# Optimization experiments

Hardware: AMD Instinct MI355X
Metric: run time of the kernel (lower is better)

## Reference

```python
import jax, jax.numpy as jnp
import numpy as np

BASE_C = 0.001
T = 0.7
MIN_RATIO = 0.5
MAX_RATIO = 2.0
EPS = 1e-7
BATCH, IN_DIM, HID, OUT_DIM = 65536, 784, 128, 10
WEIGHT_STD = 0.02


def _mobius_add(u, v, c):
    # (u +_c v) on the Poincare ball, last-dim vectors
    uv = jnp.sum(u * v, axis=-1, keepdims=True)
    uu = jnp.sum(u * u, axis=-1, keepdims=True)
    vv = jnp.sum(v * v, axis=-1, keepdims=True)
    num = (1.0 + 2.0 * c * uv + c * vv) * u + (1.0 - c * uu) * v
    den = 1.0 + 2.0 * c * uv + (c * c) * uu * vv
    return num / jnp.maximum(den, EPS)


def _mobius_scalar(x, c, r):
    # r (x)_c : tanh(r * artanh(sqrt(c)||x||)) * x / (sqrt(c)||x||)
    n = jnp.sqrt(jnp.maximum(jnp.sum(x * x, axis=-1, keepdims=True), EPS * EPS))
    sc = jnp.sqrt(c)
    arg = jnp.clip(sc * n, EPS, 1.0 - 1e-5)
    return jnp.tanh(r * jnp.arctanh(arg)) * x / (sc * n)


def poincare_ball_layer(h, u, c, t):
    # hyperbolic interpolation: ((1-t) (x)_c h) (+)_c (t (x)_c u)
    return _mobius_add(_mobius_scalar(h, c, 1.0 - t), _mobius_scalar(u, c, t), c)


def setup_inputs() -> dict:
    key = jax.random.key(0)
    ks = jax.random.split(key, 4)
    x = jax.random.normal(ks[0], (BATCH, IN_DIM), dtype=jnp.float32)
    weights1 = WEIGHT_STD * jax.random.normal(ks[1], (IN_DIM, HID), dtype=jnp.float32)
    bias1 = jnp.zeros((HID,), dtype=jnp.float32)
    weights2 = WEIGHT_STD * jax.random.normal(ks[2], (HID, HID), dtype=jnp.float32)
    bias2 = jnp.zeros((HID,), dtype=jnp.float32)
    out_weights = WEIGHT_STD * jax.random.normal(ks[3], (HID, OUT_DIM), dtype=jnp.float32)
    out_bias = jnp.zeros((OUT_DIM,), dtype=jnp.float32)
    curvature_scale = jnp.ones((1,), dtype=jnp.float32)
    return {"x": x, "weights1": weights1, "bias1": bias1, "weights2": weights2,
            "bias2": bias2, "out_weights": out_weights, "out_bias": out_bias,
            "curvature_scale": curvature_scale}


def reference(x, weights1, bias1, weights2, bias2, out_weights, out_bias, curvature_scale):
    x_flat = x.reshape(x.shape[0], -1)
    h = jnp.tanh(x_flat @ weights1 + bias1)            # [B, HID]
    u = jax.nn.sigmoid(h @ weights2 + bias2)           # [B, HID]
    # torch uses .item() -> curvature scale is detached from autodiff
    s = jax.lax.stop_gradient(jax.nn.sigmoid(curvature_scale[0]))
    adaptive_c = BASE_C * (MIN_RATIO + (MAX_RATIO - MIN_RATIO) * s)
    z = poincare_ball_layer(h, u, adaptive_c, T)
    z = jnp.where(jnp.any(jnp.isnan(z)), h, z)         # NaN fallback
    return z @ out_weights + out_bias
```

## Files before the change

kernel.cpp:

```cpp
#include <hip/hip_runtime.h>

typedef __attribute__((ext_vector_type(8))) short short8;
typedef __attribute__((ext_vector_type(4))) short short4v;
typedef __attribute__((ext_vector_type(4))) float f32x4;

#define BATCH 65536
#define IN_DIM 784
#define HID 128
#define OUT_DIM 10
#define KPAD 800
#define NKS 25
#define BM 128
#define NBLK (BATCH / BM)

#define OFF_W1H 0
#define OFF_W1L 204800
#define OFF_W2S 409600
#define OFF_W3S 442368

__device__ __forceinline__ unsigned short bf16_rne(float f) {
    unsigned u = __float_as_uint(f);
    return (unsigned short)((u + 0x7FFFu + ((u >> 16) & 1u)) >> 16);
}
__device__ __forceinline__ float fast_tanh(float x) {
    float e = __expf(2.0f * x);
    return 1.0f - 2.0f / (e + 1.0f);
}

__global__ void prep_kernel(const float* __restrict__ W1, const float* __restrict__ W2,
                            const float* __restrict__ W3,
                            unsigned short* __restrict__ w1h, unsigned short* __restrict__ w1l,
                            unsigned short* __restrict__ w2s, unsigned short* __restrict__ w3s) {
    int b = blockIdx.x, t = threadIdx.x;
    if (b < HID) {
        int col = b;
        for (int k = t; k < KPAD; k += 256) {
            float v = (k < IN_DIM) ? W1[k * HID + col] : 0.0f;
            unsigned u = __float_as_uint(v);
            unsigned short hi = (unsigned short)(u >> 16);
            float hif = __uint_as_float(u & 0xFFFF0000u);
            unsigned short lo = bf16_rne(v - hif);
            int idx = ((k >> 5) * HID + col) * 32 + (k & 31);
            w1h[idx] = hi; w1l[idx] = lo;
        }
    } else if (b == HID) {
        for (int i = t; i < HID * HID; i += 256) {
            int n = i >> 7, k = i & 127;
            w2s[i] = bf16_rne(W2[k * HID + n]);
        }
    } else {
        for (int i = t; i < 16 * HID; i += 256) {
            int j = i >> 7, k = i & 127;
            float v = (j < OUT_DIM) ? W3[k * OUT_DIM + j] : 0.0f;
            w3s[i] = bf16_rne(v);
        }
    }
}

__launch_bounds__(256, 2)
__global__ void fused_kernel(const float* __restrict__ X,
                             const float* __restrict__ b1,
                             const float* __restrict__ b2,
                             const float* __restrict__ ob,
                             const float* __restrict__ csc,
                             const unsigned short* __restrict__ w1h,
                             const unsigned short* __restrict__ w1l,
                             const unsigned short* __restrict__ w2s,
                             const unsigned short* __restrict__ w3s,
                             float* __restrict__ OUT) {
    __shared__ float xs[BM][36];
    __shared__ unsigned short w1hS[HID][40];
    __shared__ unsigned short w1lS[HID][40];
    __shared__ unsigned short ht[HID][136];

    const int t = threadIdx.x;
    const int wid = t >> 6, lane = t & 63;
    const int lg = lane >> 4, lr = lane & 15;
    const int row0 = blockIdx.x * BM;

    const float cs = csc[0];
    const float sgc = 1.0f / (1.0f + __expf(-cs));
    const float c = 0.001f * (0.5f + 1.5f * sgc);
    const float sc = sqrtf(c);

    f32x4 acc[2][8];
    #pragma unroll
    for (int f = 0; f < 8; ++f) {
        float bv = b1[16 * f + lr];
        f32x4 v = {bv, bv, bv, bv};
        acc[0][f] = v; acc[1][f] = v;
    }

    const int srow = t >> 1;
    const int shalf = t & 1;
    const float* xg = X + (size_t)(row0 + srow) * IN_DIM + shalf * 16;

    for (int ks = 0; ks < NKS; ++ks) {
        __syncthreads();
        {
            int k0 = ks * 32;
            f32x4 v0 = {0,0,0,0}, v1 = v0, v2 = v0, v3 = v0;
            if (k0 + shalf * 16 < IN_DIM) {
                const f32x4* p = (const f32x4*)(xg + k0);
                v0 = p[0]; v1 = p[1]; v2 = p[2]; v3 = p[3];
            }
            f32x4* q = (f32x4*)(&xs[srow][shalf * 16]);
            q[0] = v0; q[1] = v1; q[2] = v2; q[3] = v3;
        }
        {
            const short8* gh = (const short8*)(w1h + (ks * HID + srow) * 32 + shalf * 16);
            const short8* gl = (const short8*)(w1l + (ks * HID + srow) * 32 + shalf * 16);
            short8 h0 = gh[0], h1 = gh[1], l0 = gl[0], l1 = gl[1];
            short8* qh = (short8*)(&w1hS[srow][shalf * 16]);
            short8* ql = (short8*)(&w1lS[srow][shalf * 16]);
            qh[0] = h0; qh[1] = h1; ql[0] = l0; ql[1] = l1;
        }
        __syncthreads();

        short8 xh[2], xl[2];
        #pragma unroll
        for (int rf = 0; rf < 2; ++rf) {
            const int r = wid * 32 + rf * 16 + lr;
            const f32x4* p = (const f32x4*)(&xs[r][8 * lg]);
            f32x4 a = p[0], b = p[1];
            short8 h8, l8;
            #pragma unroll
            for (int j = 0; j < 8; ++j) {
                float v = (j < 4) ? a[j] : b[j - 4];
                unsigned u = __float_as_uint(v);
                h8[j] = (short)(u >> 16);
                float lof = v - __uint_as_float(u & 0xFFFF0000u);
                l8[j] = (short)(__float_as_uint(lof) >> 16);
            }
            xh[rf] = h8; xl[rf] = l8;
        }
        #pragma unroll
        for (int f = 0; f < 8; ++f) {
            const short8 bh = *(const short8*)(&w1hS[16 * f + lr][8 * lg]);
            const short8 bl = *(const short8*)(&w1lS[16 * f + lr][8 * lg]);
            acc[0][f] = __builtin_amdgcn_mfma_f32_16x16x32_bf16(xh[0], bh, acc[0][f], 0, 0, 0);
            acc[1][f] = __builtin_amdgcn_mfma_f32_16x16x32_bf16(xh[1], bh, acc[1][f], 0, 0, 0);
            acc[0][f] = __builtin_amdgcn_mfma_f32_16x16x32_bf16(xl[0], bh, acc[0][f], 0, 0, 0);
            acc[1][f] = __builtin_amdgcn_mfma_f32_16x16x32_bf16(xl[1], bh, acc[1][f], 0, 0, 0);
            acc[0][f] = __builtin_amdgcn_mfma_f32_16x16x32_bf16(xh[0], bl, acc[0][f], 0, 0, 0);
            acc[1][f] = __builtin_amdgcn_mfma_f32_16x16x32_bf16(xh[1], bl, acc[1][f], 0, 0, 0);
        }
    }

    #pragma unroll
    for (int rf = 0; rf < 2; ++rf) {
        const int rbase = wid * 32 + rf * 16 + 4 * lg;
        #pragma unroll
        for (int f = 0; f < 8; ++f) {
            short4v pk;
            #pragma unroll
            for (int r = 0; r < 4; ++r) {
                float h = fast_tanh(acc[rf][f][r]);
                acc[rf][f][r] = h;
                pk[r] = (short)bf16_rne(h);
            }
            *(short4v*)(&ht[16 * f + lr][rbase]) = pk;
        }
    }

    f32x4 uacc[2][8];
    #pragma unroll
    for (int f = 0; f < 8; ++f) {
        float bv = b2[16 * f + lr];
        f32x4 v = {bv, bv, bv, bv};
        uacc[0][f] = v; uacc[1][f] = v;
    }
    #pragma unroll
    for (int ks2 = 0; ks2 < 4; ++ks2) {
        short8 a2[2];
        #pragma unroll
        for (int rf = 0; rf < 2; ++rf) {
            const int rbl = wid * 32 + rf * 16 + lr;
            #pragma unroll
            for (int i = 0; i < 8; ++i)
                a2[rf][i] = (short)ht[ks2 * 32 + 8 * lg + i][rbl];
        }
        #pragma unroll
        for (int f = 0; f < 8; ++f) {
            const short8 bb = *(const short8*)(w2s + (16 * f + lr) * HID + ks2 * 32 + 8 * lg);
            uacc[0][f] = __builtin_amdgcn_mfma_f32_16x16x32_bf16(a2[0], bb, uacc[0][f], 0, 0, 0);
            uacc[1][f] = __builtin_amdgcn_mfma_f32_16x16x32_bf16(a2[1], bb, uacc[1][f], 0, 0, 0);
        }
    }
    #pragma unroll
    for (int rf = 0; rf < 2; ++rf)
        #pragma unroll
        for (int f = 0; f < 8; ++f)
            #pragma unroll
            for (int r = 0; r < 4; ++r)
                uacc[rf][f][r] = 1.0f / (1.0f + __expf(-uacc[rf][f][r]));

    float cA[2][4], cB[2][4];
    #pragma unroll
    for (int rf = 0; rf < 2; ++rf) {
        float hh[4] = {0,0,0,0}, uu[4] = {0,0,0,0}, hu[4] = {0,0,0,0};
        #pragma unroll
        for (int f = 0; f < 8; ++f)
            #pragma unroll
            for (int r = 0; r < 4; ++r) {
                float h = acc[rf][f][r], u = uacc[rf][f][r];
                hh[r] += h * h; uu[r] += u * u; hu[r] += h * u;
            }
        #pragma unroll
        for (int m = 1; m <= 8; m <<= 1)
            #pragma unroll
            for (int r = 0; r < 4; ++r) {
                hh[r] += __shfl_xor(hh[r], m);
                uu[r] += __shfl_xor(uu[r], m);
                hu[r] += __shfl_xor(hu[r], m);
            }
        #pragma unroll
        for (int r = 0; r < 4; ++r) {
            float nh = sqrtf(fmaxf(hh[r], 1e-14f));
            float nu = sqrtf(fmaxf(uu[r], 1e-14f));
            float argh = fminf(fmaxf(sc * nh, 1e-7f), 1.0f - 1e-5f);
            float argu = fminf(fmaxf(sc * nu, 1e-7f), 1.0f - 1e-5f);
            float ath = 0.5f * __logf((1.0f + argh) / (1.0f - argh));
            float atu = 0.5f * __logf((1.0f + argu) / (1.0f - argu));
            float alpha = fast_tanh(0.3f * ath) / (sc * nh);
            float beta  = fast_tanh(0.7f * atu) / (sc * nu);
            float UV = alpha * beta * hu[r];
            float UU = alpha * alpha * hh[r];
            float VV = beta * beta * uu[r];
            float den = fmaxf(1.0f + 2.0f * c * UV + c * c * UU * VV, 1e-7f);
            cA[rf][r] = (1.0f + 2.0f * c * UV + c * VV) * alpha / den;
            cB[rf][r] = (1.0f - c * UU) * beta / den;
        }
    }
    #pragma unroll
    for (int rf = 0; rf < 2; ++rf) {
        const int rbase = wid * 32 + rf * 16 + 4 * lg;
        #pragma unroll
        for (int f = 0; f < 8; ++f) {
            short4v pk;
            #pragma unroll
            for (int r = 0; r < 4; ++r) {
                float z = cA[rf][r] * acc[rf][f][r] + cB[rf][r] * uacc[rf][f][r];
                pk[r] = (short)bf16_rne(z);
            }
            *(short4v*)(&ht[16 * f + lr][rbase]) = pk;
        }
    }

    float obv = (lr < OUT_DIM) ? ob[lr] : 0.0f;
    f32x4 oacc[2];
    oacc[0][0] = obv; oacc[0][1] = obv; oacc[0][2] = obv; oacc[0][3] = obv;
    oacc[1] = oacc[0];
    #pragma unroll
    for (int ks2 = 0; ks2 < 4; ++ks2) {
        short8 a3[2];
        #pragma unroll
        for (int rf = 0; rf < 2; ++rf) {
            const int rbl = wid * 32 + rf * 16 + lr;
            #pragma unroll
            for (int i = 0; i < 8; ++i)
                a3[rf][i] = (short)ht[ks2 * 32 + 8 * lg + i][rbl];
        }
        const short8 b3 = *(const short8*)(w3s + lr * HID + ks2 * 32 + 8 * lg);
        oacc[0] = __builtin_amdgcn_mfma_f32_16x16x32_bf16(a3[0], b3, oacc[0], 0, 0, 0);
        oacc[1] = __builtin_amdgcn_mfma_f32_16x16x32_bf16(a3[1], b3, oacc[1], 0, 0, 0);
    }
    if (lr < OUT_DIM) {
        #pragma unroll
        for (int rf = 0; rf < 2; ++rf) {
            const int rbase = row0 + wid * 32 + rf * 16 + 4 * lg;
            #pragma unroll
            for (int r = 0; r < 4; ++r)
                OUT[(size_t)(rbase + r) * OUT_DIM + lr] = oacc[rf][r];
        }
    }
}

extern "C" void kernel_launch(void* const* d_in, const int* in_sizes, int n_in,
                              void* d_out, int out_size, void* d_ws, size_t ws_size,
                              hipStream_t stream) {
    const float* X  = (const float*)d_in[0];
    const float* W1 = (const float*)d_in[1];
    const float* B1 = (const float*)d_in[2];
    const float* W2 = (const float*)d_in[3];
    const float* B2 = (const float*)d_in[4];
    const float* W3 = (const float*)d_in[5];
    const float* OB = (const float*)d_in[6];
    const float* CS = (const float*)d_in[7];
    unsigned short* w1h = (unsigned short*)((char*)d_ws + OFF_W1H);
    unsigned short* w1l = (unsigned short*)((char*)d_ws + OFF_W1L);
    unsigned short* w2s = (unsigned short*)((char*)d_ws + OFF_W2S);
    unsigned short* w3s = (unsigned short*)((char*)d_ws + OFF_W3S);
    prep_kernel<<<HID + 2, 256, 0, stream>>>(W1, W2, W3, w1h, w1l, w2s, w3s);
    fused_kernel<<<NBLK, 256, 0, stream>>>(X, B1, B2, OB, CS, w1h, w1l, w2s, w3s, (float*)d_out);
}
```

Measured before the change: 328.7 us.

## Register-prefetch next K-slice and double-buffer W1 in LDS, load X directly

Rewrites the first GEMM's K loop so the next slice of X and W1 is prefetched into registers while the current slice is computed. W1 tiles go into double-buffered shared memory, which leaves one barrier per iteration instead of two. X is no longer staged through LDS: each lane loads its MFMA fragment straight from global memory. The aim is to hide global load latency and cut LDS traffic, at the cost of more registers and less coalesced X loads, with occupancy limited at 2 blocks per CU.

```diff
diff --git a/kernel.cpp b/kernel.cpp
--- a/kernel.cpp
+++ b/kernel.cpp
@@ -68,21 +68,14 @@
                              const unsigned short* __restrict__ w2s,
                              const unsigned short* __restrict__ w3s,
                              float* __restrict__ OUT) {
-    __shared__ float xs[BM][36];
-    __shared__ unsigned short w1hS[HID][40];
-    __shared__ unsigned short w1lS[HID][40];
-    __shared__ unsigned short ht[HID][136];
+    __shared__ unsigned short smem[2][2][HID][40];
+    unsigned short (*ht)[136] = (unsigned short (*)[136])&smem[0][0][0][0];
 
     const int t = threadIdx.x;
     const int wid = t >> 6, lane = t & 63;
     const int lg = lane >> 4, lr = lane & 15;
     const int row0 = blockIdx.x * BM;
 
-    const float cs = csc[0];
-    const float sgc = 1.0f / (1.0f + __expf(-cs));
-    const float c = 0.001f * (0.5f + 1.5f * sgc);
-    const float sc = sqrtf(c);
-
     f32x4 acc[2][8];
     #pragma unroll
     for (int f = 0; f < 8; ++f) {
@@ -91,42 +84,55 @@
         acc[0][f] = v; acc[1][f] = v;
     }
 
-    const int srow = t >> 1;
-    const int shalf = t & 1;
-    const float* xg = X + (size_t)(row0 + srow) * IN_DIM + shalf * 16;
+    f32x4 xcur[2][2], xnxt[2][2];
+    short8 wcur[4], wnxt[4];
+
+    #define LOADX(dst, ks)                                                        \
+        {                                                                         \
+            int k0_ = (ks) * 32 + 8 * lg;                                         \
+            _Pragma("unroll")                                                     \
+            for (int rf = 0; rf < 2; ++rf) {                                      \
+                f32x4 a_ = {0,0,0,0}, b_ = {0,0,0,0};                             \
+                if (k0_ < IN_DIM) {                                               \
+                    const f32x4* p_ = (const f32x4*)(X +                          \
+                        (size_t)(row0 + wid * 32 + rf * 16 + lr) * IN_DIM + k0_); \
+                    a_ = p_[0]; b_ = p_[1];                                       \
+                }                                                                 \
+                dst[rf][0] = a_; dst[rf][1] = b_;                                 \
+            }                                                                     \
+        }
+    #define LOADW(dst, ks)                                                        \
+        {                                                                         \
+            const short8* ph_ = (const short8*)(w1h + (ks) * 4096) + t * 2;       \
+            const short8* pl_ = (const short8*)(w1l + (ks) * 4096) + t * 2;       \
+            dst[0] = ph_[0]; dst[1] = ph_[1];                                     \
+            dst[2] = pl_[0]; dst[3] = pl_[1];                                     \
+        }
+
+    LOADX(xcur, 0);
+    LOADW(wcur, 0);
 
     for (int ks = 0; ks < NKS; ++ks) {
+        const int cur = ks & 1;
+        {
+            short8* dh = (short8*)&smem[cur][0][t >> 1][(t & 1) * 16];
+            short8* dl = (short8*)&smem[cur][1][t >> 1][(t & 1) * 16];
+            dh[0] = wcur[0]; dh[1] = wcur[1];
+            dl[0] = wcur[2]; dl[1] = wcur[3];
+        }
+        if (ks + 1 < NKS) {
+            LOADX(xnxt, ks + 1);
+            LOADW(wnxt, ks + 1);
+        }
         __syncthreads();
-        {
-            int k0 = ks * 32;
-            f32x4 v0 = {0,0,0,0}, v1 = v0, v2 = v0, v3 = v0;
-            if (k0 + shalf * 16 < IN_DIM) {
-                const f32x4* p = (const f32x4*)(xg + k0);
-                v0 = p[0]; v1 = p[1]; v2 = p[2]; v3 = p[3];
-            }
-            f32x4* q = (f32x4*)(&xs[srow][shalf * 16]);
-            q[0] = v0; q[1] = v1; q[2] = v2; q[3] = v3;
-        }
-        {
-            const short8* gh = (const short8*)(w1h + (ks * HID + srow) * 32 + shalf * 16);
-            const short8* gl = (const short8*)(w1l + (ks * HID + srow) * 32 + shalf * 16);
-            short8 h0 = gh[0], h1 = gh[1], l0 = gl[0], l1 = gl[1];
-            short8* qh = (short8*)(&w1hS[srow][shalf * 16]);
-            short8* ql = (short8*)(&w1lS[srow][shalf * 16]);
-            qh[0] = h0; qh[1] = h1; ql[0] = l0; ql[1] = l1;
-        }
-        __syncthreads();
 
         short8 xh[2], xl[2];
         #pragma unroll
         for (int rf = 0; rf < 2; ++rf) {
-            const int r = wid * 32 + rf * 16 + lr;
-            const f32x4* p = (const f32x4*)(&xs[r][8 * lg]);
-            f32x4 a = p[0], b = p[1];
             short8 h8, l8;
             #pragma unroll
             for (int j = 0; j < 8; ++j) {
-                float v = (j < 4) ? a[j] : b[j - 4];
+                float v = (j < 4) ? xcur[rf][0][j] : xcur[rf][1][j - 4];
                 unsigned u = __float_as_uint(v);
                 h8[j] = (short)(u >> 16);
                 float lof = v - __uint_as_float(u & 0xFFFF0000u);
@@ -136,8 +142,8 @@
         }
         #pragma unroll
         for (int f = 0; f < 8; ++f) {
-            const short8 bh = *(const short8*)(&w1hS[16 * f + lr][8 * lg]);
-            const short8 bl = *(const short8*)(&w1lS[16 * f + lr][8 * lg]);
+            const short8 bh = *(const short8*)&smem[cur][0][16 * f + lr][8 * lg];
+            const short8 bl = *(const short8*)&smem[cur][1][16 * f + lr][8 * lg];
             acc[0][f] = __builtin_amdgcn_mfma_f32_16x16x32_bf16(xh[0], bh, acc[0][f], 0, 0, 0);
             acc[1][f] = __builtin_amdgcn_mfma_f32_16x16x32_bf16(xh[1], bh, acc[1][f], 0, 0, 0);
             acc[0][f] = __builtin_amdgcn_mfma_f32_16x16x32_bf16(xl[0], bh, acc[0][f], 0, 0, 0);
@@ -145,7 +151,17 @@
             acc[0][f] = __builtin_amdgcn_mfma_f32_16x16x32_bf16(xh[0], bl, acc[0][f], 0, 0, 0);
             acc[1][f] = __builtin_amdgcn_mfma_f32_16x16x32_bf16(xh[1], bl, acc[1][f], 0, 0, 0);
         }
-    }
+        #pragma unroll
+        for (int rf = 0; rf < 2; ++rf) { xcur[rf][0] = xnxt[rf][0]; xcur[rf][1] = xnxt[rf][1]; }
+        #pragma unroll
+        for (int j = 0; j < 4; ++j) wcur[j] = wnxt[j];
+    }
+    __syncthreads();
+
+    const float cs = csc[0];
+    const float sgc = 1.0f / (1.0f + __expf(-cs));
+    const float c = 0.001f * (0.5f + 1.5f * sgc);
+    const float sc = sqrtf(c);
 
     #pragma unroll
     for (int rf = 0; rf < 2; ++rf) {
```

Result: no change. 327.5 us (-0.4%).
